# Performance work log

Measured on AMD Instinct MI355X. Metric: run time of the kernel, lower is better.

## Reference

```python
import jax, jax.numpy as jnp
import numpy as np
import math

B, T, C, H = 4, 2048, 1024, 16
D = C // H  # head dim = 64


def setup_inputs() -> dict:
    key = jax.random.key(0)
    k1, k2, k3, k4, k5 = jax.random.split(key, 5)
    scale = 1.0 / math.sqrt(C)
    return {
        "x": jax.random.normal(k1, (B, T, C), dtype=jnp.float32),
        "w_attn": jax.random.normal(k2, (C, 3 * C), dtype=jnp.float32) * scale,
        "b_attn": jax.random.normal(k3, (3 * C,), dtype=jnp.float32) * 0.02,
        "w_proj": jax.random.normal(k4, (C, C), dtype=jnp.float32) * scale,
        "b_proj": jax.random.normal(k5, (C,), dtype=jnp.float32) * 0.02,
    }


def reference(x, w_attn, b_attn, w_proj, b_proj):
    Bx, Tx, Cx = x.shape
    qkv = x @ w_attn + b_attn                      # [B,T,3C]
    q, k, v = jnp.split(qkv, 3, axis=-1)           # each [B,T,C]
    # reshape to [B,H,T,D]
    q = q.reshape(Bx, Tx, H, D).transpose(0, 2, 1, 3)
    k = k.reshape(Bx, Tx, H, D).transpose(0, 2, 1, 3)
    v = v.reshape(Bx, Tx, H, D).transpose(0, 2, 1, 3)
    att = jnp.einsum("bhqd,bhkd->bhqk", q, k) * (1.0 / math.sqrt(D))
    causal = jnp.tril(jnp.ones((Tx, Tx), dtype=bool))
    att = jnp.where(causal, att, -jnp.inf)
    att = jax.nn.softmax(att, axis=-1)
    y = jnp.einsum("bhqk,bhkd->bhqd", att, v)      # [B,H,T,D]
    y = y.transpose(0, 2, 1, 3).reshape(Bx, Tx, Cx)
    return y @ w_proj + b_proj
```

## Files before the change

### kernel.cpp

```cpp
#include <hip/hip_runtime.h>
#include <hip/hip_bf16.h>
#include <stdint.h>

typedef unsigned short u16;
typedef unsigned int u32;
typedef __attribute__((ext_vector_type(8))) __bf16 bf16x8;
typedef __attribute__((ext_vector_type(4))) float f32x4;
typedef __attribute__((ext_vector_type(16))) float f32x16;

#define B_ 4
#define T_ 2048
#define C_ 1024
#define H_ 16
#define D_ 64

__device__ __forceinline__ u16 f2bf(float f) {
  union { float f; u32 u; } v; v.f = f;
  u32 r = (v.u + 0x7fffu + ((v.u >> 16) & 1u)) >> 16;
  return (u16)r;
}

__device__ __forceinline__ float fexp2(float x) {
  float r;
  asm("v_exp_f32 %0, %1\n\ts_nop 0" : "=v"(r) : "v"(x));
  return r;
}

__device__ __forceinline__ u32 cvtpk(float lo, float hi2) {
  u32 r;
  asm("v_cvt_pk_bf16_f32 %0, %1, %2" : "=v"(r) : "v"(lo), "v"(hi2));
  return r;
}

__device__ __forceinline__ void gll16(const void* g, void* l) {
  __builtin_amdgcn_global_load_lds((const __attribute__((address_space(1))) void*)g,
                                   (__attribute__((address_space(3))) void*)l, 16, 0, 0);
}

__global__ void k_convert(const float* __restrict__ src, u16* __restrict__ dst, int n4) {
  int stride = gridDim.x * blockDim.x;
  for (int i = blockIdx.x * blockDim.x + threadIdx.x; i < n4; i += stride) {
    float4 v = ((const float4*)src)[i];
    ushort4 o;
    o.x = f2bf(v.x); o.y = f2bf(v.y); o.z = f2bf(v.z); o.w = f2bf(v.w);
    ((ushort4*)dst)[i] = o;
  }
}

__global__ void k_transpose_bf16(const float* __restrict__ src, u16* __restrict__ dst,
                                 int K, int N) {
  __shared__ float tile[32][33];
  int k0 = blockIdx.x * 32, n0 = blockIdx.y * 32;
  int tx = threadIdx.x, ty = threadIdx.y;
#pragma unroll
  for (int r = 0; r < 4; ++r) {
    int k = ty + r * 8;
    tile[k][tx] = src[(size_t)(k0 + k) * N + n0 + tx];
  }
  __syncthreads();
#pragma unroll
  for (int r = 0; r < 4; ++r) {
    int n = ty + r * 8;
    dst[(size_t)(n0 + n) * K + k0 + tx] = f2bf(tile[tx][n]);
  }
}

template <int MODE>
__global__ __launch_bounds__(256) void k_gemm(
    const u16* __restrict__ A, const u16* __restrict__ BT, const float* __restrict__ bias,
    float* __restrict__ outF, u16* __restrict__ qb, u16* __restrict__ kb, u16* __restrict__ vbT,
    int M, int N, int K) {
  __shared__ u16 a_lds[128 * 32];
  __shared__ u16 b_lds[128 * 32];
  const int lane = threadIdx.x & 63, wid = threadIdx.x >> 6;
  const int brow = blockIdx.y * 128, bcol = blockIdx.x * 128;
  const int wr = (wid >> 1) * 64, wc = (wid & 1) * 64;
  const int lr = lane & 15, lg = lane >> 4, lk = lg * 8;
  f32x4 acc[4][4] = {};

  for (int kt = 0; kt < K; kt += 32) {
#pragma unroll
    for (int it = 0; it < 2; ++it) {
      int cbase = (wid * 2 + it) * 64;
      int c = cbase + lane;
      int row = c >> 2, col = (c & 3) * 8;
      gll16(A + (size_t)(brow + row) * K + kt + col, &a_lds[cbase * 8]);
      gll16(BT + (size_t)(bcol + row) * K + kt + col, &b_lds[cbase * 8]);
    }
    __syncthreads();
    bf16x8 af[4], bfr[4];
#pragma unroll
    for (int m = 0; m < 4; ++m) af[m] = *(const bf16x8*)&a_lds[(wr + m * 16 + lr) * 32 + lk];
#pragma unroll
    for (int n = 0; n < 4; ++n) bfr[n] = *(const bf16x8*)&b_lds[(wc + n * 16 + lr) * 32 + lk];
#pragma unroll
    for (int m = 0; m < 4; ++m)
#pragma unroll
      for (int n = 0; n < 4; ++n)
        acc[m][n] = __builtin_amdgcn_mfma_f32_16x16x32_bf16(af[m], bfr[n], acc[m][n], 0, 0, 0);
    __syncthreads();
  }

#pragma unroll
  for (int m = 0; m < 4; ++m) {
    int row = brow + wr + m * 16 + lg * 4;
#pragma unroll
    for (int n = 0; n < 4; ++n) {
      int col = bcol + wc + n * 16 + lr;
      float bs = bias[col];
      if (MODE == 0) {
#pragma unroll
        for (int r = 0; r < 4; ++r)
          outF[(size_t)(row + r) * N + col] = acc[m][n][r] + bs;
      } else {
        int sec = col >> 10, cc = col & 1023;
        int h = cc >> 6, dd = cc & 63;
        int b = row >> 11, t = row & 2047;
        size_t bh = (size_t)(b * H_ + h);
        if (sec < 2) {
          u16* dst = (sec == 0 ? qb : kb) + (bh * T_ + t) * D_ + dd;
#pragma unroll
          for (int r = 0; r < 4; ++r) dst[(size_t)r * D_] = f2bf(acc[m][n][r] + bs);
        } else {
          ushort4 pk;
          pk.x = f2bf(acc[m][n][0] + bs);
          pk.y = f2bf(acc[m][n][1] + bs);
          pk.z = f2bf(acc[m][n][2] + bs);
          pk.w = f2bf(acc[m][n][3] + bs);
          *(ushort4*)&vbT[(bh * D_ + dd) * T_ + t] = pk;
        }
      }
    }
  }
}

__global__ __launch_bounds__(256) void k_attn(
    const u16* __restrict__ qb, const u16* __restrict__ kb,
    const u16* __restrict__ vbT, u16* __restrict__ attb) {
  __shared__ u16 kl0[64 * 64], kl1[64 * 64];
  __shared__ u16 vl0[64 * 64], vl1[64 * 64];
  const int lane = threadIdx.x & 63, wid = threadIdx.x >> 6;
  const int w = blockIdx.x;
  const int lid = (w & 7) * 64 + (w >> 3);
  const int bh = lid >> 3, qpair = lid & 7;
  const int b = bh >> 4, h = bh & 15;
  const int l31 = lane & 31, hi = lane >> 5;
  const int sw3 = l31 & 7;

  const float SC = 0.18033688f;

  const u16* kbase = kb + (size_t)bh * T_ * D_;
  const u16* vbase = vbT + (size_t)bh * D_ * T_;

  auto stage = [&](u16* kd, u16* vd, int kt) {
    const int k0 = kt * 64;
#pragma unroll
    for (int it = 0; it < 2; ++it) {
      int cbase = (wid * 2 + it) * 64;
      int c = cbase + lane;
      int cs = (c & ~7) | ((c ^ (c >> 3)) & 7);
      gll16(kbase + (size_t)k0 * D_ + (size_t)cs * 8, kd + cbase * 8);
      int vrow = cs >> 3, vcol = (cs & 7) * 8;
      gll16(vbase + (size_t)vrow * T_ + k0 + vcol, vd + cbase * 8);
    }
  };

  auto pack = [&](const f32x16& s, bf16x8* out) {
#pragma unroll
    for (int cc = 0; cc < 2; ++cc) {
      const int rb = cc * 8;
      u32 a = cvtpk(s[rb + 0], s[rb + 1]);
      u32 c = cvtpk(s[rb + 2], s[rb + 3]);
      u32 bb = cvtpk(s[rb + 4], s[rb + 5]);
      u32 d = cvtpk(s[rb + 6], s[rb + 7]);
      u32 as = __shfl_xor(a, 32, 64), cs = __shfl_xor(c, 32, 64);
      u32 bs = __shfl_xor(bb, 32, 64), ds = __shfl_xor(d, 32, 64);
      union { u32 u[4]; bf16x8 v; } t;
      t.u[0] = hi ? bs : a;
      t.u[1] = hi ? ds : c;
      t.u[2] = hi ? bb : as;
      t.u[3] = hi ? d : cs;
      out[cc] = t.v;
    }
  };

#pragma unroll 1
  for (int pass = 0; pass < 2; ++pass) {
    const int qbk = pass ? (15 - qpair) : qpair;
    const int qw = qbk * 128 + wid * 32;

    const u16* qrow = qb + ((size_t)bh * T_ + qw + l31) * D_ + hi * 8;
    bf16x8 qf[4];
#pragma unroll
    for (int j = 0; j < 4; ++j) qf[j] = *(const bf16x8*)(qrow + j * 16);

    float m = -3e38f, lsum = 0.f;
    f32x16 o0 = {}, o1 = {};

    const int nt = 2 * qbk + 2;
    const int lastkt = (qw + 31) >> 6;

    auto compute = [&](const u16* kl, const u16* vl, int kt) {
      const int k0 = kt * 64;
      f32x16 s0 = {}, s1 = {};
      __builtin_amdgcn_s_setprio(1);
#pragma unroll
      for (int j = 0; j < 4; ++j) {
        const int ch = ((2 * j + hi) ^ sw3) << 3;
        const bf16x8 kf0 = *(const bf16x8*)&kl[l31 * 64 + ch];
        const bf16x8 kf1 = *(const bf16x8*)&kl[(l31 + 32) * 64 + ch];
        s0 = __builtin_amdgcn_mfma_f32_32x32x16_bf16(kf0, qf[j], s0, 0, 0, 0);
        s1 = __builtin_amdgcn_mfma_f32_32x32x16_bf16(kf1, qf[j], s1, 0, 0, 0);
      }
      __builtin_amdgcn_s_setprio(0);

      if (kt == lastkt) {
        const int q = qw + l31;
#pragma unroll
        for (int r = 0; r < 16; ++r) {
          const int kv = k0 + (r & 3) + 8 * (r >> 2) + 4 * hi;
          if (kv > q) s0[r] = -3e38f;
          if (kv + 32 > q) s1[r] = -3e38f;
        }
      }

      float mx = s0[0];
#pragma unroll
      for (int r = 1; r < 16; ++r) mx = fmaxf(mx, s0[r]);
#pragma unroll
      for (int r = 0; r < 16; ++r) mx = fmaxf(mx, s1[r]);
      mx = fmaxf(mx, __shfl_xor(mx, 32, 64));

      if (!__all(mx <= m + 44.0f)) {
        float mn = fmaxf(m, mx);
        float f = fexp2((m - mn) * SC);
        m = mn;
        lsum *= f;
#pragma unroll
        for (int r = 0; r < 16; ++r) { o0[r] *= f; o1[r] *= f; }
      }
      const float msc = m * SC;

#pragma unroll
      for (int r = 0; r < 16; ++r) s0[r] = fexp2(fmaf(s0[r], SC, -msc));
#pragma unroll
      for (int r = 0; r < 16; ++r) s1[r] = fexp2(fmaf(s1[r], SC, -msc));

      float ps = 0.f;
#pragma unroll
      for (int r = 0; r < 16; ++r) ps += s0[r] + s1[r];
      ps += __shfl_xor(ps, 32, 64);
      lsum += ps;

      bf16x8 pb[4];
      pack(s0, &pb[0]);
      pack(s1, &pb[2]);

      __builtin_amdgcn_s_setprio(1);
#pragma unroll
      for (int c = 0; c < 4; ++c) {
        const int ch = ((2 * c + hi) ^ sw3) << 3;
        const bf16x8 vf0 = *(const bf16x8*)&vl[l31 * 64 + ch];
        const bf16x8 vf1 = *(const bf16x8*)&vl[(l31 + 32) * 64 + ch];
        o0 = __builtin_amdgcn_mfma_f32_32x32x16_bf16(vf0, pb[c], o0, 0, 0, 0);
        o1 = __builtin_amdgcn_mfma_f32_32x32x16_bf16(vf1, pb[c], o1, 0, 0, 0);
      }
      __builtin_amdgcn_s_setprio(0);
    };

    stage(kl0, vl0, 0);
    __syncthreads();
    int kt = 0;
    while (true) {
      if (kt + 1 < nt) stage(kl1, vl1, kt + 1);
      if (kt <= lastkt) compute(kl0, vl0, kt);
      __syncthreads();
      if (++kt >= nt) break;
      if (kt + 1 < nt) stage(kl0, vl0, kt + 1);
      if (kt <= lastkt) compute(kl1, vl1, kt);
      __syncthreads();
      if (++kt >= nt) break;
    }

    const float inv = 1.0f / lsum;
    u16* orow = attb + ((size_t)b * T_ + qw + l31) * C_ + h * D_;
#pragma unroll
    for (int rg = 0; rg < 4; ++rg) {
      ushort4 w0, w1;
      w0.x = f2bf(o0[rg * 4 + 0] * inv); w0.y = f2bf(o0[rg * 4 + 1] * inv);
      w0.z = f2bf(o0[rg * 4 + 2] * inv); w0.w = f2bf(o0[rg * 4 + 3] * inv);
      w1.x = f2bf(o1[rg * 4 + 0] * inv); w1.y = f2bf(o1[rg * 4 + 1] * inv);
      w1.z = f2bf(o1[rg * 4 + 2] * inv); w1.w = f2bf(o1[rg * 4 + 3] * inv);
      const int d0 = rg * 8 + hi * 4;
      *(ushort4*)(orow + d0) = w0;
      *(ushort4*)(orow + d0 + 32) = w1;
    }
  }
}

extern "C" void kernel_launch(void* const* d_in, const int* in_sizes, int n_in,
                              void* d_out, int out_size, void* d_ws, size_t ws_size,
                              hipStream_t stream) {
  const float* x = (const float*)d_in[0];
  const float* w_attn = (const float*)d_in[1];
  const float* b_attn = (const float*)d_in[2];
  const float* w_proj = (const float*)d_in[3];
  const float* b_proj = (const float*)d_in[4];
  float* out = (float*)d_out;

  char* ws = (char*)d_ws;
  const size_t MB = 1024 * 1024;
  u16* xb   = (u16*)(ws);
  u16* attb = xb;
  u16* waT  = (u16*)(ws + 16 * MB);
  u16* wpT  = (u16*)(ws + 22 * MB);
  u16* qb   = (u16*)(ws + 24 * MB);
  u16* kb   = (u16*)(ws + 40 * MB);
  u16* vbT  = (u16*)(ws + 56 * MB);

  k_convert<<<2048, 256, 0, stream>>>(x, xb, (B_ * T_ * C_) / 4);
  k_transpose_bf16<<<dim3(C_ / 32, 3 * C_ / 32), dim3(32, 8), 0, stream>>>(w_attn, waT, C_, 3 * C_);
  k_transpose_bf16<<<dim3(C_ / 32, C_ / 32), dim3(32, 8), 0, stream>>>(w_proj, wpT, C_, C_);

  k_gemm<1><<<dim3(3 * C_ / 128, (B_ * T_) / 128), 256, 0, stream>>>(
      xb, waT, b_attn, nullptr, qb, kb, vbT, B_ * T_, 3 * C_, C_);

  k_attn<<<512, 256, 0, stream>>>(qb, kb, vbT, attb);

  k_gemm<0><<<dim3(C_ / 128, (B_ * T_) / 128), 256, 0, stream>>>(
      attb, wpT, b_proj, out, nullptr, nullptr, nullptr, B_ * T_, C_, C_);
}
```

Before: 191.6 us.

## Triple-buffer GEMM LDS tiles with async prefetch two stages ahead

Replaces the single-buffered LDS staging in the GEMM kernel with a three-slot ring. Global-to-LDS loads are issued two k-tiles ahead, with vmcnt waits and one barrier per iteration instead of two. The MFMA block runs at raised wave priority. This aims to hide global load latency behind matrix math, at the cost of three times the LDS footprint, which may reduce occupancy.

Measured after the change: 182.8 us. 4.6% less time.

```diff
diff --git a/kernel.cpp b/kernel.cpp
--- a/kernel.cpp
+++ b/kernel.cpp
@@ -70,35 +70,60 @@
     const u16* __restrict__ A, const u16* __restrict__ BT, const float* __restrict__ bias,
     float* __restrict__ outF, u16* __restrict__ qb, u16* __restrict__ kb, u16* __restrict__ vbT,
     int M, int N, int K) {
-  __shared__ u16 a_lds[128 * 32];
-  __shared__ u16 b_lds[128 * 32];
+  __shared__ u16 al[3][128 * 32];
+  __shared__ u16 bl[3][128 * 32];
   const int lane = threadIdx.x & 63, wid = threadIdx.x >> 6;
   const int brow = blockIdx.y * 128, bcol = blockIdx.x * 128;
   const int wr = (wid >> 1) * 64, wc = (wid & 1) * 64;
   const int lr = lane & 15, lg = lane >> 4, lk = lg * 8;
   f32x4 acc[4][4] = {};
 
-  for (int kt = 0; kt < K; kt += 32) {
+  auto stage = [&](u16* ad, u16* bd, int t2) {
+    const int kt = t2 * 32;
 #pragma unroll
     for (int it = 0; it < 2; ++it) {
       int cbase = (wid * 2 + it) * 64;
       int c = cbase + lane;
       int row = c >> 2, col = (c & 3) * 8;
-      gll16(A + (size_t)(brow + row) * K + kt + col, &a_lds[cbase * 8]);
-      gll16(BT + (size_t)(bcol + row) * K + kt + col, &b_lds[cbase * 8]);
-    }
-    __syncthreads();
+      gll16(A + (size_t)(brow + row) * K + kt + col, ad + cbase * 8);
+      gll16(BT + (size_t)(bcol + row) * K + kt + col, bd + cbase * 8);
+    }
+  };
+
+  const int nt = K / 32;
+  stage(al[0], bl[0], 0);
+  stage(al[1], bl[1], 1);
+
+  for (int t = 0; t < nt; ++t) {
+    if (t == nt - 1) { asm volatile("s_waitcnt vmcnt(0)" ::: "memory"); }
+    else             { asm volatile("s_waitcnt vmcnt(4)" ::: "memory"); }
+    __builtin_amdgcn_sched_barrier(0);
+    __builtin_amdgcn_s_barrier();
+    __builtin_amdgcn_sched_barrier(0);
+
+    const int nxt = t + 2;
+    if (nxt < nt) {
+      const int ib = nxt % 3;
+      stage(al[ib], bl[ib], nxt);
+    }
+
+    const u16* ab = al[t % 3];
+    const u16* bb = bl[t % 3];
     bf16x8 af[4], bfr[4];
 #pragma unroll
-    for (int m = 0; m < 4; ++m) af[m] = *(const bf16x8*)&a_lds[(wr + m * 16 + lr) * 32 + lk];
-#pragma unroll
-    for (int n = 0; n < 4; ++n) bfr[n] = *(const bf16x8*)&b_lds[(wc + n * 16 + lr) * 32 + lk];
+    for (int m = 0; m < 4; ++m) af[m] = *(const bf16x8*)&ab[(wr + m * 16 + lr) * 32 + lk];
+#pragma unroll
+    for (int n = 0; n < 4; ++n) bfr[n] = *(const bf16x8*)&bb[(wc + n * 16 + lr) * 32 + lk];
+
+    asm volatile("s_waitcnt lgkmcnt(0)" ::: "memory");
+    __builtin_amdgcn_sched_barrier(0);
+    __builtin_amdgcn_s_setprio(1);
 #pragma unroll
     for (int m = 0; m < 4; ++m)
 #pragma unroll
       for (int n = 0; n < 4; ++n)
         acc[m][n] = __builtin_amdgcn_mfma_f32_16x16x32_bf16(af[m], bfr[n], acc[m][n], 0, 0, 0);
-    __syncthreads();
+    __builtin_amdgcn_s_setprio(0);
   }
 
 #pragma unroll
```
